# Performance work log

Measured on AMD Instinct MI355X. Metric: run time of the kernel, lower is better.

## Reference

```python
import jax, jax.numpy as jnp
import numpy as np

DEPTH = 3
HIDDEN = 300
ATOM_FDIM = 133
BOND_FDIM = 147


def setup_inputs() -> dict:
    key = jax.random.key(0)
    ks = jax.random.split(key, 10)
    n_atoms, n_bonds, max_nb, n_mols = 200000, 400000, 6, 10000
    f_atoms = jax.random.normal(ks[0], (n_atoms, ATOM_FDIM), dtype=jnp.float32)
    f_bonds = jax.random.normal(ks[1], (n_bonds, BOND_FDIM), dtype=jnp.float32)
    a2b = jax.random.randint(ks[2], (n_atoms, max_nb), 0, n_bonds)
    b2a = jax.random.randint(ks[3], (n_bonds,), 0, n_atoms)
    b2revb = jax.random.randint(ks[4], (n_bonds,), 0, n_bonds)
    # learned parameters (fan-in scaled)
    W_i = jax.random.normal(ks[5], (BOND_FDIM, HIDDEN), dtype=jnp.float32) / np.sqrt(BOND_FDIM)
    W_h = jax.random.normal(ks[6], (HIDDEN, HIDDEN), dtype=jnp.float32) / np.sqrt(HIDDEN)
    W_o = jax.random.normal(ks[7], (ATOM_FDIM + HIDDEN, HIDDEN), dtype=jnp.float32) / np.sqrt(ATOM_FDIM + HIDDEN)
    b_o = jnp.zeros((HIDDEN,), dtype=jnp.float32)
    return {"f_atoms": f_atoms, "f_bonds": f_bonds, "a2b": a2b, "b2a": b2a,
            "b2revb": b2revb, "W_i": W_i, "W_h": W_h, "W_o": W_o, "b_o": b_o,
            "n_mols": n_mols}


def reference(f_atoms, f_bonds, a2b, b2a, b2revb, W_i, W_h, W_o, b_o, n_mols):
    act = jax.nn.relu
    # input = W_i(f_bonds); message = act(input)
    inp = f_bonds @ W_i                       # [n_bonds, H]
    message = act(inp)
    for _ in range(DEPTH - 1):
        nei_a_message = message[a2b]          # [n_atoms, max_nb, H] gather
        a_message = nei_a_message.sum(axis=1)  # [n_atoms, H]
        rev_message = message[b2revb]         # [n_bonds, H]
        message = a_message[b2a] - rev_message
        message = act(inp + message @ W_h)
    # final atom readout
    a_message = message[a2b].sum(axis=1)      # [n_atoms, H]
    a_input = jnp.concatenate([f_atoms, a_message], axis=1)
    atom_hiddens = act(a_input @ W_o + b_o)   # [n_atoms, H]
    # scope-based mean pooling (uniform molecules: n_atoms = n_mols * apm)
    apm = f_atoms.shape[0] // n_mols
    mol_vecs = atom_hiddens.reshape(n_mols, apm, HIDDEN).mean(axis=1)
    return mol_vecs
```

## Files before the change

kernel.cpp:

```cpp
#include <hip/hip_runtime.h>
#include <hip/hip_bf16.h>
#include <cstdint>
#include <cstddef>

#define HP 320

typedef unsigned short ushortT;
typedef __attribute__((ext_vector_type(8))) __bf16 bf16x8;
typedef __attribute__((ext_vector_type(4))) float f32x4;

__device__ __forceinline__ float b2f(unsigned u) {
    union { unsigned i; float f; } v; v.i = u << 16; return v.f;
}
__device__ __forceinline__ ushortT f2b(float f) {
    union { float f; unsigned i; } v; v.f = f;
    unsigned x = v.i;
    return (ushortT)((x + 0x7fffu + ((x >> 16) & 1u)) >> 16);
}
__device__ __forceinline__ unsigned subpk(unsigned a, unsigned r) {
    union { unsigned i; float f; } al, ah, rl, rh;
    al.i = a << 16; ah.i = a & 0xffff0000u;
    rl.i = r << 16; rh.i = r & 0xffff0000u;
    float lo = al.f - rl.f, hi = ah.f - rh.f;
    return (unsigned)f2b(lo) | ((unsigned)f2b(hi) << 16);
}
__device__ __forceinline__ uint4 subpk4(uint4 a, uint4 r) {
    uint4 o;
    o.x = subpk(a.x, r.x); o.y = subpk(a.y, r.y);
    o.z = subpk(a.z, r.z); o.w = subpk(a.w, r.w);
    return o;
}

__device__ __forceinline__ void pack_one(int idx, const float* __restrict__ W,
                                         int Ksrc, ushortT* __restrict__ dst) {
    int j = idx & 7, col = (idx >> 3) & 15, kg = (idx >> 7) & 3;
    int t = idx >> 9; int nt = t % 20, kt = t / 20;
    int k = kt * 32 + kg * 8 + j, n = nt * 16 + col;
    float v = (k < Ksrc && n < 300) ? W[k * 300 + n] : 0.f;
    dst[idx] = f2b(v);
}
__device__ __forceinline__ void pack_wo(int idx, const float* __restrict__ W,
                                        ushortT* __restrict__ dst) {
    int j = idx & 7, col = (idx >> 3) & 15, kg = (idx >> 7) & 3;
    int t = idx >> 9; int nt = t % 20, kt = t / 20;
    int k = kt * 32 + kg * 8 + j, n = nt * 16 + col;
    int src = (k < 133) ? k : ((k >= 160 && k < 460) ? (k - 27) : -1);
    float v = (src >= 0 && n < 300) ? W[src * 300 + n] : 0.f;
    dst[idx] = f2b(v);
}

__global__ __launch_bounds__(256) void k_pack_weights(
    const float* __restrict__ Wi, const float* __restrict__ Wh,
    const float* __restrict__ Wo, const float* __restrict__ bo,
    ushortT* __restrict__ Wipk, ushortT* __restrict__ Whpk,
    ushortT* __restrict__ Wopk, float* __restrict__ bop) {
    int idx = blockIdx.x * 256 + threadIdx.x;
    if (idx < 51200)  pack_one(idx, Wi, 147, Wipk);
    if (idx < 102400) pack_one(idx, Wh, 300, Whpk);
    if (idx < 153600) pack_wo(idx, Wo, Wopk);
    if (idx < HP) bop[idx] = (idx < 300) ? bo[idx] : 0.f;
}

template <int FD>
__global__ __launch_bounds__(256) void k_pack_feat(
    const float* __restrict__ src, ushortT* __restrict__ dst, int nrows) {
    int t = blockIdx.x * 256 + threadIdx.x;
    if (t >= nrows * 20) return;
    int row = t / 20, q = t - row * 20;
    int k0 = q * 8;
    union { ushortT u[8]; uint4 v; } o;
#pragma unroll
    for (int j = 0; j < 8; j++) {
        int k = k0 + j;
        o.u[j] = (k < FD) ? f2b(src[(size_t)row * FD + k]) : (ushortT)0;
    }
    *(uint4*)(dst + (size_t)row * 160 + k0) = o.v;
}

template <int MODE, bool AUXP>
__global__ __launch_bounds__(256, 3) void k_mfma(
    const float* __restrict__ fa, const float* __restrict__ fb,
    const ushortT* __restrict__ aux,
    const ushortT* __restrict__ amsg, const ushortT* __restrict__ msgin,
    const int* __restrict__ b2a, const int* __restrict__ b2revb,
    const ushortT* __restrict__ Bpk1, const ushortT* __restrict__ Bpk2,
    const float* __restrict__ bop,
    ushortT* __restrict__ outp) {
    constexpr int KT = (MODE == 0) ? 5 : 15;
    constexpr int SPLIT = (MODE == 1) ? 10 : KT;
    constexpr int SP = 328;
    __shared__ __align__(16) ushortT panel[(MODE == 1) ? 64 * SP : 8];

    const int tid = threadIdx.x, wave = tid >> 6, lane = tid & 63;
    const int row0 = blockIdx.x * 64;
    const int wm = wave >> 1, wn = wave & 1;
    const int growA = row0 + wm * 32 + (lane & 15);
    const int kg8 = (lane >> 4) * 8;

    if (MODE == 1) {
#pragma unroll
        for (int it = 0; it < 10; it++) {
            int flat = tid + 256 * it;
            int row = flat / 40, ch = flat - row * 40;
            size_t oa = (size_t)b2a[row0 + row] * HP;
            size_t orv = (size_t)b2revb[row0 + row] * HP;
            uint4 ua = *(const uint4*)(amsg + oa + ch * 8);
            uint4 ur = *(const uint4*)(msgin + orv + ch * 8);
            *(uint4*)&panel[row * SP + ch * 8] = subpk4(ua, ur);
        }
        __syncthreads();
    }

    f32x4 acc[2][10];
#pragma unroll
    for (int i = 0; i < 2; i++)
#pragma unroll
        for (int n = 0; n < 10; n++) acc[i][n] = (f32x4){0.f, 0.f, 0.f, 0.f};

    uint4 breg[2][5];
    uint4 apre[2][2];
    const int boff = (wn * 10) * 512 + (lane >> 4) * 128 + (lane & 15) * 8;

#define LOADB_H(kt, h, buf)                                                          \
    {                                                                                \
        const ushortT* bp = ((kt) < SPLIT) ? (Bpk1 + (size_t)(kt) * 10240)           \
                                           : (Bpk2 + (size_t)((kt) - SPLIT) * 10240);\
        _Pragma("unroll")                                                            \
        for (int n = 0; n < 5; n++)                                                  \
            breg[buf][n] = *(const uint4*)(bp + boff + ((h) * 5 + n) * 512);         \
    }

    auto LOADA = [&](int kt, int buf) {
        if (MODE == 1) {
            int k0 = (kt - 10) * 32 + kg8;
            if (AUXP) {
                apre[buf][0] = *(const uint4*)(aux + (size_t)growA * 160 + k0);
                apre[buf][1] = *(const uint4*)(aux + (size_t)(growA + 16) * 160 + k0);
            } else {
                union { ushortT u[8]; uint4 v; } t0, t1;
#pragma unroll
                for (int j = 0; j < 8; j++) {
                    int k = k0 + j;
                    t0.u[j] = (k < 147) ? f2b(fb[(size_t)growA * 147 + k]) : (ushortT)0;
                    t1.u[j] = (k < 147) ? f2b(fb[(size_t)(growA + 16) * 147 + k]) : (ushortT)0;
                }
                apre[buf][0] = t0.v; apre[buf][1] = t1.v;
            }
        } else if (MODE == 0) {
            int k0 = kt * 32 + kg8;
            if (AUXP) {
                apre[buf][0] = *(const uint4*)(aux + (size_t)growA * 160 + k0);
                apre[buf][1] = *(const uint4*)(aux + (size_t)(growA + 16) * 160 + k0);
            } else {
                union { ushortT u[8]; uint4 v; } t0, t1;
#pragma unroll
                for (int j = 0; j < 8; j++) {
                    int k = k0 + j;
                    t0.u[j] = (k < 147) ? f2b(fb[(size_t)growA * 147 + k]) : (ushortT)0;
                    t1.u[j] = (k < 147) ? f2b(fb[(size_t)(growA + 16) * 147 + k]) : (ushortT)0;
                }
                apre[buf][0] = t0.v; apre[buf][1] = t1.v;
            }
        } else {
            int k0 = kt * 32 + kg8;
            if (kt >= 5) {
                apre[buf][0] = *(const uint4*)(amsg + (size_t)growA * HP + (k0 - 160));
                apre[buf][1] = *(const uint4*)(amsg + (size_t)(growA + 16) * HP + (k0 - 160));
            } else if (AUXP) {
                apre[buf][0] = *(const uint4*)(aux + (size_t)growA * 160 + k0);
                apre[buf][1] = *(const uint4*)(aux + (size_t)(growA + 16) * 160 + k0);
            } else {
                union { ushortT u[8]; uint4 v; } t0, t1;
#pragma unroll
                for (int j = 0; j < 8; j++) {
                    int k = k0 + j;
                    t0.u[j] = (k < 133) ? f2b(fa[(size_t)growA * 133 + k]) : (ushortT)0;
                    t1.u[j] = (k < 133) ? f2b(fa[(size_t)(growA + 16) * 133 + k]) : (ushortT)0;
                }
                apre[buf][0] = t0.v; apre[buf][1] = t1.v;
            }
        }
    };

    LOADB_H(0, 0, 0);
    if (MODE != 1) LOADA(0, 0);
#pragma unroll
    for (int kt = 0; kt < KT; kt++) {
        LOADB_H(kt, 1, 1);
        if (kt + 1 < KT && (MODE != 1 || kt + 1 >= 10))
            LOADA(kt + 1, (kt + 1) & 1);
        bf16x8 a0, a1;
        if (MODE != 1 || kt >= 10) {
            *(uint4*)&a0 = apre[kt & 1][0];
            *(uint4*)&a1 = apre[kt & 1][1];
        } else {
            const int k0 = kt * 32 + kg8;
            a0 = *(bf16x8*)&panel[(wm * 32 + (lane & 15)) * SP + k0];
            a1 = *(bf16x8*)&panel[(wm * 32 + 16 + (lane & 15)) * SP + k0];
        }
#pragma unroll
        for (int n = 0; n < 5; n++) {
            bf16x8 b;
            *(uint4*)&b = breg[0][n];
            acc[0][n] = __builtin_amdgcn_mfma_f32_16x16x32_bf16(b, a0, acc[0][n], 0, 0, 0);
            acc[1][n] = __builtin_amdgcn_mfma_f32_16x16x32_bf16(b, a1, acc[1][n], 0, 0, 0);
        }
        if (kt + 1 < KT) LOADB_H(kt + 1, 0, 0);
#pragma unroll
        for (int n = 0; n < 5; n++) {
            bf16x8 b;
            *(uint4*)&b = breg[1][n];
            acc[0][5 + n] = __builtin_amdgcn_mfma_f32_16x16x32_bf16(b, a0, acc[0][5 + n], 0, 0, 0);
            acc[1][5 + n] = __builtin_amdgcn_mfma_f32_16x16x32_bf16(b, a1, acc[1][5 + n], 0, 0, 0);
        }
    }
#undef LOADB_H

#pragma unroll
    for (int i = 0; i < 2; i++) {
        size_t gr = (size_t)(row0 + wm * 32 + i * 16 + (lane & 15));
#pragma unroll
        for (int n = 0; n < 10; n++) {
            int col = wn * 160 + n * 16 + (lane >> 4) * 4;
            float4 v = make_float4(acc[i][n][0], acc[i][n][1], acc[i][n][2], acc[i][n][3]);
            if (MODE == 2) {
                float4 bias = *(const float4*)&bop[col];
                v.x += bias.x; v.y += bias.y; v.z += bias.z; v.w += bias.w;
            }
            ushort4 u;
            u.x = f2b(fmaxf(v.x, 0.f)); u.y = f2b(fmaxf(v.y, 0.f));
            u.z = f2b(fmaxf(v.z, 0.f)); u.w = f2b(fmaxf(v.w, 0.f));
            *(ushort4*)&outp[gr * HP + col] = u;
        }
    }
}

__global__ __launch_bounds__(256) void k_atom_sum(
    const ushortT* __restrict__ msg, const int* __restrict__ a2b,
    ushortT* __restrict__ amsg, int nA) {
    int t = blockIdx.x * 256 + threadIdx.x;
    int a = t / 40, q = t - a * 40;
    if (a >= nA) return;
    float s[8];
#pragma unroll
    for (int e = 0; e < 8; e++) s[e] = 0.f;
#pragma unroll
    for (int j = 0; j < 6; j++) {
        int b = a2b[a * 6 + j];
        uint4 u = *(const uint4*)(msg + (size_t)b * HP + q * 8);
        s[0] += b2f(u.x & 0xffff); s[1] += b2f(u.x >> 16);
        s[2] += b2f(u.y & 0xffff); s[3] += b2f(u.y >> 16);
        s[4] += b2f(u.z & 0xffff); s[5] += b2f(u.z >> 16);
        s[6] += b2f(u.w & 0xffff); s[7] += b2f(u.w >> 16);
    }
    uint4 o;
    o.x = (unsigned)f2b(s[0]) | ((unsigned)f2b(s[1]) << 16);
    o.y = (unsigned)f2b(s[2]) | ((unsigned)f2b(s[3]) << 16);
    o.z = (unsigned)f2b(s[4]) | ((unsigned)f2b(s[5]) << 16);
    o.w = (unsigned)f2b(s[6]) | ((unsigned)f2b(s[7]) << 16);
    *(uint4*)(amsg + (size_t)a * HP + q * 8) = o;
}

__global__ __launch_bounds__(256) void k_pool(
    const ushortT* __restrict__ ah, float* __restrict__ out, int n_mols, int apm) {
    int t = blockIdx.x * 256 + threadIdx.x;
    int m = t / 75, c4 = t - m * 75;
    if (m >= n_mols) return;
    float4 s = make_float4(0, 0, 0, 0);
    for (int u = 0; u < apm; u++) {
        ushort4 q = *(const ushort4*)&ah[(size_t)(m * apm + u) * HP + c4 * 4];
        s.x += b2f(q.x); s.y += b2f(q.y); s.z += b2f(q.z); s.w += b2f(q.w);
    }
    float inv = 1.0f / (float)apm;
    s.x *= inv; s.y *= inv; s.z *= inv; s.w *= inv;
    *(float4*)&out[(size_t)m * 300 + c4 * 4] = s;
}

extern "C" void kernel_launch(void* const* d_in, const int* in_sizes, int n_in,
                              void* d_out, int out_size, void* d_ws, size_t ws_size,
                              hipStream_t stream) {
    const float* fa     = (const float*)d_in[0];
    const float* fb     = (const float*)d_in[1];
    const int*   a2b    = (const int*)d_in[2];
    const int*   b2a    = (const int*)d_in[3];
    const int*   b2revb = (const int*)d_in[4];
    const float* Wi     = (const float*)d_in[5];
    const float* Wh     = (const float*)d_in[6];
    const float* Wo     = (const float*)d_in[7];
    const float* bo     = (const float*)d_in[8];

    const int nA     = in_sizes[0] / 133;
    const int nB     = in_sizes[1] / 147;
    const int n_mols = out_size / 300;
    const int apm    = nA / n_mols;

    char* p = (char*)d_ws;
    ushortT* Wipk = (ushortT*)p;  p += (size_t)51200 * 2;
    ushortT* Whpk = (ushortT*)p;  p += (size_t)102400 * 2;
    ushortT* Wopk = (ushortT*)p;  p += (size_t)153600 * 2;
    float*   bop  = (float*)p;    p += (size_t)HP * 4;
    p = (char*)(((uintptr_t)p + 255) & ~(uintptr_t)255);

    const size_t msgBytes  = (size_t)nB * HP * 2;
    const size_t amsgBytes = (size_t)nA * HP * 2;
    const size_t fbbBytes  = (size_t)nB * 160 * 2;
    const size_t faaBytes  = (size_t)nA * 160 * 2;
    const size_t headBytes = (size_t)(p - (char*)d_ws);
    const size_t baseNeed  = headBytes + 2 * msgBytes + amsgBytes;
    const bool use_fbb = ws_size >= baseNeed + fbbBytes;
    const bool use_faa = ws_size >= baseNeed + fbbBytes + faaBytes;

    ushortT* msgA = (ushortT*)p;  p += msgBytes;
    ushortT* msgB = (ushortT*)p;  p += msgBytes;
    ushortT* amsg = (ushortT*)p;  p += amsgBytes;
    ushortT* fbb  = use_fbb ? (ushortT*)p : nullptr;  p += use_fbb ? fbbBytes : 0;
    ushortT* faa  = use_faa ? (ushortT*)p : nullptr;
    ushortT* ah   = msgB;
    float*   out  = (float*)d_out;

    k_pack_weights<<<600, 256, 0, stream>>>(Wi, Wh, Wo, bo, Wipk, Whpk, Wopk, bop);
    if (use_fbb)
        k_pack_feat<147><<<(nB * 20 + 255) / 256, 256, 0, stream>>>(fb, fbb, nB);
    if (use_faa)
        k_pack_feat<133><<<(nA * 20 + 255) / 256, 256, 0, stream>>>(fa, faa, nA);

    const int asum_grid = (int)(((size_t)nA * 40 + 255) / 256);

    if (use_fbb)
        k_mfma<0, true ><<<nB / 64, 256, 0, stream>>>(fa, fb, fbb, nullptr, nullptr, nullptr, nullptr,
                                                      Wipk, Wipk, bop, msgA);
    else
        k_mfma<0, false><<<nB / 64, 256, 0, stream>>>(fa, fb, nullptr, nullptr, nullptr, nullptr, nullptr,
                                                      Wipk, Wipk, bop, msgA);

    k_atom_sum<<<asum_grid, 256, 0, stream>>>(msgA, a2b, amsg, nA);
    if (use_fbb)
        k_mfma<1, true ><<<nB / 64, 256, 0, stream>>>(fa, fb, fbb, amsg, msgA, b2a, b2revb,
                                                      Whpk, Wipk, bop, msgB);
    else
        k_mfma<1, false><<<nB / 64, 256, 0, stream>>>(fa, fb, nullptr, amsg, msgA, b2a, b2revb,
                                                      Whpk, Wipk, bop, msgB);

    k_atom_sum<<<asum_grid, 256, 0, stream>>>(msgB, a2b, amsg, nA);
    if (use_fbb)
        k_mfma<1, true ><<<nB / 64, 256, 0, stream>>>(fa, fb, fbb, amsg, msgB, b2a, b2revb,
                                                      Whpk, Wipk, bop, msgA);
    else
        k_mfma<1, false><<<nB / 64, 256, 0, stream>>>(fa, fb, nullptr, amsg, msgB, b2a, b2revb,
                                                      Whpk, Wipk, bop, msgA);

    k_atom_sum<<<asum_grid, 256, 0, stream>>>(msgA, a2b, amsg, nA);
    if (use_faa)
        k_mfma<2, true ><<<nA / 64, 256, 0, stream>>>(fa, fb, faa, amsg, nullptr, nullptr, nullptr,
                                                      Wopk, Wopk, bop, ah);
    else
        k_mfma<2, false><<<nA / 64, 256, 0, stream>>>(fa, fb, nullptr, amsg, nullptr, nullptr, nullptr,
                                                      Wopk, Wopk, bop, ah);
    k_pool<<<((n_mols * 75) + 255) / 256, 256, 0, stream>>>(ah, out, n_mols, apm);
}
```

Before: 1.630 ms.

## Apply W_h before neighbor aggregation by exploiting linearity of the message update

Rewrites each message-passing step as P = message @ W_h followed by atom summation over P and a gather-and-subtract epilogue (amsg[b2a] - P[b2revb]) fused into an f_bonds @ W_i GEMM with ReLU. This removes the LDS panel build, its __syncthreads and the gather-before-GEMM prologue in the bond kernel. In exchange it adds a separate GEMM pass per depth, with an extra full write and read of a bond-sized bf16 intermediate. It also changes rounding, because the projected messages are rounded to bf16 before being summed and differenced.

```diff
diff --git a/kernel.cpp b/kernel.cpp
--- a/kernel.cpp
+++ b/kernel.cpp
@@ -16,19 +16,6 @@
     union { float f; unsigned i; } v; v.f = f;
     unsigned x = v.i;
     return (ushortT)((x + 0x7fffu + ((x >> 16) & 1u)) >> 16);
-}
-__device__ __forceinline__ unsigned subpk(unsigned a, unsigned r) {
-    union { unsigned i; float f; } al, ah, rl, rh;
-    al.i = a << 16; ah.i = a & 0xffff0000u;
-    rl.i = r << 16; rh.i = r & 0xffff0000u;
-    float lo = al.f - rl.f, hi = ah.f - rh.f;
-    return (unsigned)f2b(lo) | ((unsigned)f2b(hi) << 16);
-}
-__device__ __forceinline__ uint4 subpk4(uint4 a, uint4 r) {
-    uint4 o;
-    o.x = subpk(a.x, r.x); o.y = subpk(a.y, r.y);
-    o.z = subpk(a.z, r.z); o.w = subpk(a.w, r.w);
-    return o;
 }
 
 __device__ __forceinline__ void pack_one(int idx, const float* __restrict__ W,
@@ -81,15 +68,12 @@
 __global__ __launch_bounds__(256, 3) void k_mfma(
     const float* __restrict__ fa, const float* __restrict__ fb,
     const ushortT* __restrict__ aux,
-    const ushortT* __restrict__ amsg, const ushortT* __restrict__ msgin,
+    const ushortT* __restrict__ amsg,
+    const ushortT* __restrict__ msgin,
     const int* __restrict__ b2a, const int* __restrict__ b2revb,
-    const ushortT* __restrict__ Bpk1, const ushortT* __restrict__ Bpk2,
-    const float* __restrict__ bop,
+    const ushortT* __restrict__ Bpk, const float* __restrict__ bop,
     ushortT* __restrict__ outp) {
-    constexpr int KT = (MODE == 0) ? 5 : 15;
-    constexpr int SPLIT = (MODE == 1) ? 10 : KT;
-    constexpr int SP = 328;
-    __shared__ __align__(16) ushortT panel[(MODE == 1) ? 64 * SP : 8];
+    constexpr int KT = (MODE == 3) ? 10 : ((MODE == 2) ? 15 : 5);
 
     const int tid = threadIdx.x, wave = tid >> 6, lane = tid & 63;
     const int row0 = blockIdx.x * 64;
@@ -97,18 +81,13 @@
     const int growA = row0 + wm * 32 + (lane & 15);
     const int kg8 = (lane >> 4) * 8;
 
-    if (MODE == 1) {
-#pragma unroll
-        for (int it = 0; it < 10; it++) {
-            int flat = tid + 256 * it;
-            int row = flat / 40, ch = flat - row * 40;
-            size_t oa = (size_t)b2a[row0 + row] * HP;
-            size_t orv = (size_t)b2revb[row0 + row] * HP;
-            uint4 ua = *(const uint4*)(amsg + oa + ch * 8);
-            uint4 ur = *(const uint4*)(msgin + orv + ch * 8);
-            *(uint4*)&panel[row * SP + ch * 8] = subpk4(ua, ur);
-        }
-        __syncthreads();
+    int ia[2], ir[2];
+    if (MODE == 4) {
+#pragma unroll
+        for (int i = 0; i < 2; i++) {
+            ia[i] = b2a[growA + 16 * i];
+            ir[i] = b2revb[growA + 16 * i];
+        }
     }
 
     f32x4 acc[2][10];
@@ -121,48 +100,20 @@
     uint4 apre[2][2];
     const int boff = (wn * 10) * 512 + (lane >> 4) * 128 + (lane & 15) * 8;
 
-#define LOADB_H(kt, h, buf)                                                          \
-    {                                                                                \
-        const ushortT* bp = ((kt) < SPLIT) ? (Bpk1 + (size_t)(kt) * 10240)           \
-                                           : (Bpk2 + (size_t)((kt) - SPLIT) * 10240);\
-        _Pragma("unroll")                                                            \
-        for (int n = 0; n < 5; n++)                                                  \
-            breg[buf][n] = *(const uint4*)(bp + boff + ((h) * 5 + n) * 512);         \
+#define LOADB_H(kt, h, buf)                                                  \
+    {                                                                        \
+        const ushortT* bp = Bpk + (size_t)(kt) * 10240;                      \
+        _Pragma("unroll")                                                    \
+        for (int n = 0; n < 5; n++)                                          \
+            breg[buf][n] = *(const uint4*)(bp + boff + ((h) * 5 + n) * 512); \
     }
 
     auto LOADA = [&](int kt, int buf) {
-        if (MODE == 1) {
-            int k0 = (kt - 10) * 32 + kg8;
-            if (AUXP) {
-                apre[buf][0] = *(const uint4*)(aux + (size_t)growA * 160 + k0);
-                apre[buf][1] = *(const uint4*)(aux + (size_t)(growA + 16) * 160 + k0);
-            } else {
-                union { ushortT u[8]; uint4 v; } t0, t1;
-#pragma unroll
-                for (int j = 0; j < 8; j++) {
-                    int k = k0 + j;
-                    t0.u[j] = (k < 147) ? f2b(fb[(size_t)growA * 147 + k]) : (ushortT)0;
-                    t1.u[j] = (k < 147) ? f2b(fb[(size_t)(growA + 16) * 147 + k]) : (ushortT)0;
-                }
-                apre[buf][0] = t0.v; apre[buf][1] = t1.v;
-            }
-        } else if (MODE == 0) {
-            int k0 = kt * 32 + kg8;
-            if (AUXP) {
-                apre[buf][0] = *(const uint4*)(aux + (size_t)growA * 160 + k0);
-                apre[buf][1] = *(const uint4*)(aux + (size_t)(growA + 16) * 160 + k0);
-            } else {
-                union { ushortT u[8]; uint4 v; } t0, t1;
-#pragma unroll
-                for (int j = 0; j < 8; j++) {
-                    int k = k0 + j;
-                    t0.u[j] = (k < 147) ? f2b(fb[(size_t)growA * 147 + k]) : (ushortT)0;
-                    t1.u[j] = (k < 147) ? f2b(fb[(size_t)(growA + 16) * 147 + k]) : (ushortT)0;
-                }
-                apre[buf][0] = t0.v; apre[buf][1] = t1.v;
-            }
-        } else {
-            int k0 = kt * 32 + kg8;
+        int k0 = kt * 32 + kg8;
+        if (MODE == 3) {
+            apre[buf][0] = *(const uint4*)(msgin + (size_t)growA * HP + k0);
+            apre[buf][1] = *(const uint4*)(msgin + (size_t)(growA + 16) * HP + k0);
+        } else if (MODE == 2) {
             if (kt >= 5) {
                 apre[buf][0] = *(const uint4*)(amsg + (size_t)growA * HP + (k0 - 160));
                 apre[buf][1] = *(const uint4*)(amsg + (size_t)(growA + 16) * HP + (k0 - 160));
@@ -179,25 +130,32 @@
                 }
                 apre[buf][0] = t0.v; apre[buf][1] = t1.v;
             }
+        } else {
+            if (AUXP) {
+                apre[buf][0] = *(const uint4*)(aux + (size_t)growA * 160 + k0);
+                apre[buf][1] = *(const uint4*)(aux + (size_t)(growA + 16) * 160 + k0);
+            } else {
+                union { ushortT u[8]; uint4 v; } t0, t1;
+#pragma unroll
+                for (int j = 0; j < 8; j++) {
+                    int k = k0 + j;
+                    t0.u[j] = (k < 147) ? f2b(fb[(size_t)growA * 147 + k]) : (ushortT)0;
+                    t1.u[j] = (k < 147) ? f2b(fb[(size_t)(growA + 16) * 147 + k]) : (ushortT)0;
+                }
+                apre[buf][0] = t0.v; apre[buf][1] = t1.v;
+            }
         }
     };
 
     LOADB_H(0, 0, 0);
-    if (MODE != 1) LOADA(0, 0);
+    LOADA(0, 0);
 #pragma unroll
     for (int kt = 0; kt < KT; kt++) {
         LOADB_H(kt, 1, 1);
-        if (kt + 1 < KT && (MODE != 1 || kt + 1 >= 10))
-            LOADA(kt + 1, (kt + 1) & 1);
+        if (kt + 1 < KT) LOADA(kt + 1, (kt + 1) & 1);
         bf16x8 a0, a1;
-        if (MODE != 1 || kt >= 10) {
-            *(uint4*)&a0 = apre[kt & 1][0];
-            *(uint4*)&a1 = apre[kt & 1][1];
-        } else {
-            const int k0 = kt * 32 + kg8;
-            a0 = *(bf16x8*)&panel[(wm * 32 + (lane & 15)) * SP + k0];
-            a1 = *(bf16x8*)&panel[(wm * 32 + 16 + (lane & 15)) * SP + k0];
-        }
+        *(uint4*)&a0 = apre[kt & 1][0];
+        *(uint4*)&a1 = apre[kt & 1][1];
 #pragma unroll
         for (int n = 0; n < 5; n++) {
             bf16x8 b;
@@ -219,6 +177,8 @@
 #pragma unroll
     for (int i = 0; i < 2; i++) {
         size_t gr = (size_t)(row0 + wm * 32 + i * 16 + (lane & 15));
+        const ushortT* pa = (MODE == 4) ? (amsg + (size_t)ia[i] * HP) : nullptr;
+        const ushortT* pr = (MODE == 4) ? (msgin + (size_t)ir[i] * HP) : nullptr;
 #pragma unroll
         for (int n = 0; n < 10; n++) {
             int col = wn * 160 + n * 16 + (lane >> 4) * 4;
@@ -227,9 +187,21 @@
                 float4 bias = *(const float4*)&bop[col];
                 v.x += bias.x; v.y += bias.y; v.z += bias.z; v.w += bias.w;
             }
+            if (MODE == 4) {
+                ushort4 qa = *(const ushort4*)&pa[col];
+                ushort4 qr = *(const ushort4*)&pr[col];
+                v.x += b2f(qa.x) - b2f(qr.x);
+                v.y += b2f(qa.y) - b2f(qr.y);
+                v.z += b2f(qa.z) - b2f(qr.z);
+                v.w += b2f(qa.w) - b2f(qr.w);
+            }
             ushort4 u;
-            u.x = f2b(fmaxf(v.x, 0.f)); u.y = f2b(fmaxf(v.y, 0.f));
-            u.z = f2b(fmaxf(v.z, 0.f)); u.w = f2b(fmaxf(v.w, 0.f));
+            if (MODE == 3) {
+                u.x = f2b(v.x); u.y = f2b(v.y); u.z = f2b(v.z); u.w = f2b(v.w);
+            } else {
+                u.x = f2b(fmaxf(v.x, 0.f)); u.y = f2b(fmaxf(v.y, 0.f));
+                u.z = f2b(fmaxf(v.z, 0.f)); u.w = f2b(fmaxf(v.w, 0.f));
+            }
             *(ushort4*)&outp[gr * HP + col] = u;
         }
     }
@@ -325,36 +297,33 @@
         k_pack_feat<133><<<(nA * 20 + 255) / 256, 256, 0, stream>>>(fa, faa, nA);
 
     const int asum_grid = (int)(((size_t)nA * 40 + 255) / 256);
+    const int gB = nB / 64, gA = nA / 64;
 
     if (use_fbb)
-        k_mfma<0, true ><<<nB / 64, 256, 0, stream>>>(fa, fb, fbb, nullptr, nullptr, nullptr, nullptr,
-                                                      Wipk, Wipk, bop, msgA);
+        k_mfma<0, true ><<<gB, 256, 0, stream>>>(fa, fb, fbb, nullptr, nullptr, nullptr, nullptr,
+                                                 Wipk, bop, msgA);
     else
-        k_mfma<0, false><<<nB / 64, 256, 0, stream>>>(fa, fb, nullptr, nullptr, nullptr, nullptr, nullptr,
-                                                      Wipk, Wipk, bop, msgA);
-
-    k_atom_sum<<<asum_grid, 256, 0, stream>>>(msgA, a2b, amsg, nA);
-    if (use_fbb)
-        k_mfma<1, true ><<<nB / 64, 256, 0, stream>>>(fa, fb, fbb, amsg, msgA, b2a, b2revb,
-                                                      Whpk, Wipk, bop, msgB);
-    else
-        k_mfma<1, false><<<nB / 64, 256, 0, stream>>>(fa, fb, nullptr, amsg, msgA, b2a, b2revb,
-                                                      Whpk, Wipk, bop, msgB);
-
-    k_atom_sum<<<asum_grid, 256, 0, stream>>>(msgB, a2b, amsg, nA);
-    if (use_fbb)
-        k_mfma<1, true ><<<nB / 64, 256, 0, stream>>>(fa, fb, fbb, amsg, msgB, b2a, b2revb,
-                                                      Whpk, Wipk, bop, msgA);
-    else
-        k_mfma<1, false><<<nB / 64, 256, 0, stream>>>(fa, fb, nullptr, amsg, msgB, b2a, b2revb,
-                                                      Whpk, Wipk, bop, msgA);
+        k_mfma<0, false><<<gB, 256, 0, stream>>>(fa, fb, nullptr, nullptr, nullptr, nullptr, nullptr,
+                                                 Wipk, bop, msgA);
+
+    for (int d = 0; d < 2; d++) {
+        k_mfma<3, true><<<gB, 256, 0, stream>>>(fa, fb, nullptr, nullptr, msgA, nullptr, nullptr,
+                                                Whpk, bop, msgB);
+        k_atom_sum<<<asum_grid, 256, 0, stream>>>(msgB, a2b, amsg, nA);
+        if (use_fbb)
+            k_mfma<4, true ><<<gB, 256, 0, stream>>>(fa, fb, fbb, amsg, msgB, b2a, b2revb,
+                                                     Wipk, bop, msgA);
+        else
+            k_mfma<4, false><<<gB, 256, 0, stream>>>(fa, fb, nullptr, amsg, msgB, b2a, b2revb,
+                                                     Wipk, bop, msgA);
+    }
 
     k_atom_sum<<<asum_grid, 256, 0, stream>>>(msgA, a2b, amsg, nA);
     if (use_faa)
-        k_mfma<2, true ><<<nA / 64, 256, 0, stream>>>(fa, fb, faa, amsg, nullptr, nullptr, nullptr,
-                                                      Wopk, Wopk, bop, ah);
+        k_mfma<2, true ><<<gA, 256, 0, stream>>>(fa, fb, faa, amsg, nullptr, nullptr, nullptr,
+                                                 Wopk, bop, ah);
     else
-        k_mfma<2, false><<<nA / 64, 256, 0, stream>>>(fa, fb, nullptr, amsg, nullptr, nullptr, nullptr,
-                                                      Wopk, Wopk, bop, ah);
+        k_mfma<2, false><<<gA, 256, 0, stream>>>(fa, fb, nullptr, amsg, nullptr, nullptr, nullptr,
+                                                 Wopk, bop, ah);
     k_pool<<<((n_mols * 75) + 255) / 256, 256, 0, stream>>>(ah, out, n_mols, apm);
 }
```

Result: slower. 2.136 ms (+31.0%).

## Stream gathered message A-operands directly into registers instead of LDS panel

Applied to the files above, without the earlier changes.

The message-update GEMM used to gather (amsg[b2a] - msg[b2revb]) for the whole 64-row tile into an LDS panel behind a block barrier before any MFMA ran. Now each lane gathers its own A fragments per k-step into double-buffered registers and does the subtraction just before the MFMA, so the gather overlaps with compute and the LDS and barrier go away. s_setprio hints are also added around the MFMA groups. The trade-off is more live registers and row-scattered loads inside the main loop, where each 16-byte load now comes from a random row per lane.

```diff
diff --git a/kernel.cpp b/kernel.cpp
--- a/kernel.cpp
+++ b/kernel.cpp
@@ -88,8 +88,6 @@
     ushortT* __restrict__ outp) {
     constexpr int KT = (MODE == 0) ? 5 : 15;
     constexpr int SPLIT = (MODE == 1) ? 10 : KT;
-    constexpr int SP = 328;
-    __shared__ __align__(16) ushortT panel[(MODE == 1) ? 64 * SP : 8];
 
     const int tid = threadIdx.x, wave = tid >> 6, lane = tid & 63;
     const int row0 = blockIdx.x * 64;
@@ -97,18 +95,12 @@
     const int growA = row0 + wm * 32 + (lane & 15);
     const int kg8 = (lane >> 4) * 8;
 
+    size_t offa0 = 0, offr0 = 0, offa1 = 0, offr1 = 0;
     if (MODE == 1) {
-#pragma unroll
-        for (int it = 0; it < 10; it++) {
-            int flat = tid + 256 * it;
-            int row = flat / 40, ch = flat - row * 40;
-            size_t oa = (size_t)b2a[row0 + row] * HP;
-            size_t orv = (size_t)b2revb[row0 + row] * HP;
-            uint4 ua = *(const uint4*)(amsg + oa + ch * 8);
-            uint4 ur = *(const uint4*)(msgin + orv + ch * 8);
-            *(uint4*)&panel[row * SP + ch * 8] = subpk4(ua, ur);
-        }
-        __syncthreads();
+        offa0 = (size_t)b2a[growA] * HP;
+        offr0 = (size_t)b2revb[growA] * HP;
+        offa1 = (size_t)b2a[growA + 16] * HP;
+        offr1 = (size_t)b2revb[growA + 16] * HP;
     }
 
     f32x4 acc[2][10];
@@ -118,7 +110,8 @@
         for (int n = 0; n < 10; n++) acc[i][n] = (f32x4){0.f, 0.f, 0.f, 0.f};
 
     uint4 breg[2][5];
-    uint4 apre[2][2];
+    uint4 ga[2][2];
+    uint4 gr[2][2];
     const int boff = (wn * 10) * 512 + (lane >> 4) * 128 + (lane & 15) * 8;
 
 #define LOADB_H(kt, h, buf)                                                          \
@@ -132,10 +125,51 @@
 
     auto LOADA = [&](int kt, int buf) {
         if (MODE == 1) {
-            int k0 = (kt - 10) * 32 + kg8;
+            if (kt < 10) {
+                int k0 = kt * 32 + kg8;
+                ga[buf][0] = *(const uint4*)(amsg + offa0 + k0);
+                gr[buf][0] = *(const uint4*)(msgin + offr0 + k0);
+                ga[buf][1] = *(const uint4*)(amsg + offa1 + k0);
+                gr[buf][1] = *(const uint4*)(msgin + offr1 + k0);
+            } else {
+                int k0 = (kt - 10) * 32 + kg8;
+                if (AUXP) {
+                    ga[buf][0] = *(const uint4*)(aux + (size_t)growA * 160 + k0);
+                    ga[buf][1] = *(const uint4*)(aux + (size_t)(growA + 16) * 160 + k0);
+                } else {
+                    union { ushortT u[8]; uint4 v; } t0, t1;
+#pragma unroll
+                    for (int j = 0; j < 8; j++) {
+                        int k = k0 + j;
+                        t0.u[j] = (k < 147) ? f2b(fb[(size_t)growA * 147 + k]) : (ushortT)0;
+                        t1.u[j] = (k < 147) ? f2b(fb[(size_t)(growA + 16) * 147 + k]) : (ushortT)0;
+                    }
+                    ga[buf][0] = t0.v; ga[buf][1] = t1.v;
+                }
+            }
+        } else if (MODE == 2) {
+            int k0 = kt * 32 + kg8;
+            if (kt >= 5) {
+                ga[buf][0] = *(const uint4*)(amsg + (size_t)growA * HP + (k0 - 160));
+                ga[buf][1] = *(const uint4*)(amsg + (size_t)(growA + 16) * HP + (k0 - 160));
+            } else if (AUXP) {
+                ga[buf][0] = *(const uint4*)(aux + (size_t)growA * 160 + k0);
+                ga[buf][1] = *(const uint4*)(aux + (size_t)(growA + 16) * 160 + k0);
+            } else {
+                union { ushortT u[8]; uint4 v; } t0, t1;
+#pragma unroll
+                for (int j = 0; j < 8; j++) {
+                    int k = k0 + j;
+                    t0.u[j] = (k < 133) ? f2b(fa[(size_t)growA * 133 + k]) : (ushortT)0;
+                    t1.u[j] = (k < 133) ? f2b(fa[(size_t)(growA + 16) * 133 + k]) : (ushortT)0;
+                }
+                ga[buf][0] = t0.v; ga[buf][1] = t1.v;
+            }
+        } else {
+            int k0 = kt * 32 + kg8;
             if (AUXP) {
-                apre[buf][0] = *(const uint4*)(aux + (size_t)growA * 160 + k0);
-                apre[buf][1] = *(const uint4*)(aux + (size_t)(growA + 16) * 160 + k0);
+                ga[buf][0] = *(const uint4*)(aux + (size_t)growA * 160 + k0);
+                ga[buf][1] = *(const uint4*)(aux + (size_t)(growA + 16) * 160 + k0);
             } else {
                 union { ushortT u[8]; uint4 v; } t0, t1;
 #pragma unroll
@@ -144,60 +178,28 @@
                     t0.u[j] = (k < 147) ? f2b(fb[(size_t)growA * 147 + k]) : (ushortT)0;
                     t1.u[j] = (k < 147) ? f2b(fb[(size_t)(growA + 16) * 147 + k]) : (ushortT)0;
                 }
-                apre[buf][0] = t0.v; apre[buf][1] = t1.v;
+                ga[buf][0] = t0.v; ga[buf][1] = t1.v;
             }
-        } else if (MODE == 0) {
-            int k0 = kt * 32 + kg8;
-            if (AUXP) {
-                apre[buf][0] = *(const uint4*)(aux + (size_t)growA * 160 + k0);
-                apre[buf][1] = *(const uint4*)(aux + (size_t)(growA + 16) * 160 + k0);
-            } else {
-                union { ushortT u[8]; uint4 v; } t0, t1;
-#pragma unroll
-                for (int j = 0; j < 8; j++) {
-                    int k = k0 + j;
-                    t0.u[j] = (k < 147) ? f2b(fb[(size_t)growA * 147 + k]) : (ushortT)0;
-                    t1.u[j] = (k < 147) ? f2b(fb[(size_t)(growA + 16) * 147 + k]) : (ushortT)0;
-                }
-                apre[buf][0] = t0.v; apre[buf][1] = t1.v;
-            }
-        } else {
-            int k0 = kt * 32 + kg8;
-            if (kt >= 5) {
-                apre[buf][0] = *(const uint4*)(amsg + (size_t)growA * HP + (k0 - 160));
-                apre[buf][1] = *(const uint4*)(amsg + (size_t)(growA + 16) * HP + (k0 - 160));
-            } else if (AUXP) {
-                apre[buf][0] = *(const uint4*)(aux + (size_t)growA * 160 + k0);
-                apre[buf][1] = *(const uint4*)(aux + (size_t)(growA + 16) * 160 + k0);
-            } else {
-                union { ushortT u[8]; uint4 v; } t0, t1;
-#pragma unroll
-                for (int j = 0; j < 8; j++) {
-                    int k = k0 + j;
-                    t0.u[j] = (k < 133) ? f2b(fa[(size_t)growA * 133 + k]) : (ushortT)0;
-                    t1.u[j] = (k < 133) ? f2b(fa[(size_t)(growA + 16) * 133 + k]) : (ushortT)0;
-                }
-                apre[buf][0] = t0.v; apre[buf][1] = t1.v;
-            }
         }
     };
 
     LOADB_H(0, 0, 0);
-    if (MODE != 1) LOADA(0, 0);
+    LOADA(0, 0);
 #pragma unroll
     for (int kt = 0; kt < KT; kt++) {
         LOADB_H(kt, 1, 1);
-        if (kt + 1 < KT && (MODE != 1 || kt + 1 >= 10))
-            LOADA(kt + 1, (kt + 1) & 1);
+        if (kt + 1 < KT) LOADA(kt + 1, (kt + 1) & 1);
         bf16x8 a0, a1;
-        if (MODE != 1 || kt >= 10) {
-            *(uint4*)&a0 = apre[kt & 1][0];
-            *(uint4*)&a1 = apre[kt & 1][1];
+        if (MODE == 1 && kt < 10) {
+            uint4 d0 = subpk4(ga[kt & 1][0], gr[kt & 1][0]);
+            uint4 d1 = subpk4(ga[kt & 1][1], gr[kt & 1][1]);
+            *(uint4*)&a0 = d0;
+            *(uint4*)&a1 = d1;
         } else {
-            const int k0 = kt * 32 + kg8;
-            a0 = *(bf16x8*)&panel[(wm * 32 + (lane & 15)) * SP + k0];
-            a1 = *(bf16x8*)&panel[(wm * 32 + 16 + (lane & 15)) * SP + k0];
-        }
+            *(uint4*)&a0 = ga[kt & 1][0];
+            *(uint4*)&a1 = ga[kt & 1][1];
+        }
+        __builtin_amdgcn_s_setprio(1);
 #pragma unroll
         for (int n = 0; n < 5; n++) {
             bf16x8 b;
@@ -205,7 +207,9 @@
             acc[0][n] = __builtin_amdgcn_mfma_f32_16x16x32_bf16(b, a0, acc[0][n], 0, 0, 0);
             acc[1][n] = __builtin_amdgcn_mfma_f32_16x16x32_bf16(b, a1, acc[1][n], 0, 0, 0);
         }
+        __builtin_amdgcn_s_setprio(0);
         if (kt + 1 < KT) LOADB_H(kt + 1, 0, 0);
+        __builtin_amdgcn_s_setprio(1);
 #pragma unroll
         for (int n = 0; n < 5; n++) {
             bf16x8 b;
@@ -213,12 +217,13 @@
             acc[0][5 + n] = __builtin_amdgcn_mfma_f32_16x16x32_bf16(b, a0, acc[0][5 + n], 0, 0, 0);
             acc[1][5 + n] = __builtin_amdgcn_mfma_f32_16x16x32_bf16(b, a1, acc[1][5 + n], 0, 0, 0);
         }
+        __builtin_amdgcn_s_setprio(0);
     }
 #undef LOADB_H
 
 #pragma unroll
     for (int i = 0; i < 2; i++) {
-        size_t gr = (size_t)(row0 + wm * 32 + i * 16 + (lane & 15));
+        size_t gr2 = (size_t)(row0 + wm * 32 + i * 16 + (lane & 15));
 #pragma unroll
         for (int n = 0; n < 10; n++) {
             int col = wn * 160 + n * 16 + (lane >> 4) * 4;
@@ -230,7 +235,7 @@
             ushort4 u;
             u.x = f2b(fmaxf(v.x, 0.f)); u.y = f2b(fmaxf(v.y, 0.f));
             u.z = f2b(fmaxf(v.z, 0.f)); u.w = f2b(fmaxf(v.w, 0.f));
-            *(ushort4*)&outp[gr * HP + col] = u;
+            *(ushort4*)&outp[gr2 * HP + col] = u;
         }
     }
 }
@@ -325,36 +330,37 @@
         k_pack_feat<133><<<(nA * 20 + 255) / 256, 256, 0, stream>>>(fa, faa, nA);
 
     const int asum_grid = (int)(((size_t)nA * 40 + 255) / 256);
+    const int gB = nB / 64, gA = nA / 64;
 
     if (use_fbb)
-        k_mfma<0, true ><<<nB / 64, 256, 0, stream>>>(fa, fb, fbb, nullptr, nullptr, nullptr, nullptr,
-                                                      Wipk, Wipk, bop, msgA);
+        k_mfma<0, true ><<<gB, 256, 0, stream>>>(fa, fb, fbb, nullptr, nullptr, nullptr, nullptr,
+                                                 Wipk, Wipk, bop, msgA);
     else
-        k_mfma<0, false><<<nB / 64, 256, 0, stream>>>(fa, fb, nullptr, nullptr, nullptr, nullptr, nullptr,
-                                                      Wipk, Wipk, bop, msgA);
+        k_mfma<0, false><<<gB, 256, 0, stream>>>(fa, fb, nullptr, nullptr, nullptr, nullptr, nullptr,
+                                                 Wipk, Wipk, bop, msgA);
 
     k_atom_sum<<<asum_grid, 256, 0, stream>>>(msgA, a2b, amsg, nA);
     if (use_fbb)
-        k_mfma<1, true ><<<nB / 64, 256, 0, stream>>>(fa, fb, fbb, amsg, msgA, b2a, b2revb,
-                                                      Whpk, Wipk, bop, msgB);
+        k_mfma<1, true ><<<gB, 256, 0, stream>>>(fa, fb, fbb, amsg, msgA, b2a, b2revb,
+                                                 Whpk, Wipk, bop, msgB);
     else
-        k_mfma<1, false><<<nB / 64, 256, 0, stream>>>(fa, fb, nullptr, amsg, msgA, b2a, b2revb,
-                                                      Whpk, Wipk, bop, msgB);
+        k_mfma<1, false><<<gB, 256, 0, stream>>>(fa, fb, nullptr, amsg, msgA, b2a, b2revb,
+                                                 Whpk, Wipk, bop, msgB);
 
     k_atom_sum<<<asum_grid, 256, 0, stream>>>(msgB, a2b, amsg, nA);
     if (use_fbb)
-        k_mfma<1, true ><<<nB / 64, 256, 0, stream>>>(fa, fb, fbb, amsg, msgB, b2a, b2revb,
-                                                      Whpk, Wipk, bop, msgA);
+        k_mfma<1, true ><<<gB, 256, 0, stream>>>(fa, fb, fbb, amsg, msgB, b2a, b2revb,
+                                                 Whpk, Wipk, bop, msgA);
     else
-        k_mfma<1, false><<<nB / 64, 256, 0, stream>>>(fa, fb, nullptr, amsg, msgB, b2a, b2revb,
-                                                      Whpk, Wipk, bop, msgA);
+        k_mfma<1, false><<<gB, 256, 0, stream>>>(fa, fb, nullptr, amsg, msgB, b2a, b2revb,
+                                                 Whpk, Wipk, bop, msgA);
 
     k_atom_sum<<<asum_grid, 256, 0, stream>>>(msgA, a2b, amsg, nA);
     if (use_faa)
-        k_mfma<2, true ><<<nA / 64, 256, 0, stream>>>(fa, fb, faa, amsg, nullptr, nullptr, nullptr,
-                                                      Wopk, Wopk, bop, ah);
+        k_mfma<2, true ><<<gA, 256, 0, stream>>>(fa, fb, faa, amsg, nullptr, nullptr, nullptr,
+                                                 Wopk, Wopk, bop, ah);
     else
-        k_mfma<2, false><<<nA / 64, 256, 0, stream>>>(fa, fb, nullptr, amsg, nullptr, nullptr, nullptr,
-                                                      Wopk, Wopk, bop, ah);
+        k_mfma<2, false><<<gA, 256, 0, stream>>>(fa, fb, nullptr, amsg, nullptr, nullptr, nullptr,
+                                                 Wopk, Wopk, bop, ah);
     k_pool<<<((n_mols * 75) + 255) / 256, 256, 0, stream>>>(ah, out, n_mols, apm);
 }
```

After: 1.996 ms. 1.22x slower.
